# Optimization experiments

Hardware: AMD Instinct MI355X
Metric: run time of the kernel (lower is better)

## Reference

```python
import jax, jax.numpy as jnp
import numpy as np

NUM_HEADS = 16


def setup_inputs() -> dict:
    key = jax.random.key(0)
    ks = jax.random.split(key, 5)
    B, S, E = 4, 2048, 1024
    scale = 1.0 / np.sqrt(E)
    return {
        "x": jax.random.normal(ks[0], (B, S, E), dtype=jnp.float32),
        "w_in": jax.random.normal(ks[1], (E, 3 * E), dtype=jnp.float32) * scale,
        "b_in": jax.random.normal(ks[2], (3 * E,), dtype=jnp.float32) * 0.02,
        "w_out": jax.random.normal(ks[3], (E, E), dtype=jnp.float32) * scale,
        "b_out": jax.random.normal(ks[4], (E,), dtype=jnp.float32) * 0.02,
    }


def reference(x, w_in, b_in, w_out, b_out):
    B, S, E = x.shape
    H = NUM_HEADS
    D = E // H  # head dim
    qkv = x @ w_in + b_in                      # [B,S,3E]
    q, k, v = jnp.split(qkv, 3, axis=-1)       # each [B,S,E]
    q = q.reshape(B, S, H, D)
    k = k.reshape(B, S, H, D)
    v = v.reshape(B, S, H, D)
    # scores scaled by 1/sqrt(D); note: original's causal masked_fill is a
    # no-op (not in-place), so attention is unmasked.
    scores = jnp.einsum("bqhd,bkhd->bhqk", q, k) / jnp.sqrt(jnp.float32(D))
    attn = jax.nn.softmax(scores, axis=-1)      # [B,H,S,S]
    out = jnp.einsum("bhqk,bkhd->bqhd", attn, v).reshape(B, S, E)
    return out @ w_out + b_out
```

## Files before the change

### kernel.cpp

```cpp
#include <hip/hip_runtime.h>
#include <math.h>

#define B_ 4
#define S_ 2048
#define E_ 1024
#define H_ 16
#define D_ 64
#define M_ (B_ * S_)

using f32x4  = __attribute__((ext_vector_type(4))) float;
using short8 = __attribute__((ext_vector_type(8))) short;
using half8  = __attribute__((ext_vector_type(8))) _Float16;
using ushort8_t = __attribute__((ext_vector_type(8))) unsigned short;

__device__ inline unsigned short f2h(float f) {
    _Float16 h = (_Float16)f;
    unsigned short u; __builtin_memcpy(&u, &h, 2); return u;
}
__device__ inline void splith(float f, unsigned short& ho, unsigned short& lo) {
    _Float16 h = (_Float16)f;
    float hf = (float)h;
    _Float16 l = (_Float16)(f - hf);
    __builtin_memcpy(&ho, &h, 2);
    __builtin_memcpy(&lo, &l, 2);
}
__device__ inline unsigned pk2h(float a, float b) {
    auto t = __builtin_amdgcn_cvt_pkrtz(a, b);
    unsigned u; __builtin_memcpy(&u, &t, 4); return u;
}
__device__ inline float ex2(float x) {
#if __has_builtin(__builtin_amdgcn_exp2f)
    return __builtin_amdgcn_exp2f(x);
#else
    return exp2f(x);
#endif
}
__device__ inline f32x4 mfma16(short8 a, short8 b, f32x4 c) {
    half8 ha, hb;
    __builtin_memcpy(&ha, &a, 16);
    __builtin_memcpy(&hb, &b, 16);
    return __builtin_amdgcn_mfma_f32_16x16x32_f16(ha, hb, c, 0, 0, 0);
}
__device__ inline void gload_lds16(const void* g, void* l) {
    __builtin_amdgcn_global_load_lds(
        (const __attribute__((address_space(1))) void*)g,
        (__attribute__((address_space(3))) void*)l, 16, 0, 0);
}

#define QSCALE 0.18033688f

__global__ __launch_bounds__(256)
void split_f16_kernel(const float* __restrict__ X,
                      unsigned short* __restrict__ Xh,
                      unsigned short* __restrict__ Xl)
{
    const size_t i = ((size_t)blockIdx.x * 256 + threadIdx.x) * 4;
    float4 v = *(const float4*)(X + i);
    ushort4 h, l;
    splith(v.x, h.x, l.x);
    splith(v.y, h.y, l.y);
    splith(v.z, h.z, l.z);
    splith(v.w, h.w, l.w);
    *(ushort4*)(Xh + i) = h;
    *(ushort4*)(Xl + i) = l;
}

__global__ __launch_bounds__(256)
void transpose_cvt_kernel(const float* __restrict__ W,
                          unsigned short* __restrict__ Th, int R, int C)
{
    __shared__ float t[32][33];
    const int tx = threadIdx.x & 31, ty = threadIdx.x >> 5;
    const int c0 = blockIdx.x * 32, r0 = blockIdx.y * 32;
    #pragma unroll
    for (int i = 0; i < 4; ++i)
        t[ty + 8 * i][tx] = W[(size_t)(r0 + ty + 8 * i) * C + c0 + tx];
    __syncthreads();
    #pragma unroll
    for (int i = 0; i < 4; ++i) {
        float v = t[tx][ty + 8 * i];
        Th[(size_t)(c0 + ty + 8 * i) * R + r0 + tx] = f2h(v);
    }
}

template<int OUT_MODE>
__global__ __launch_bounds__(256)
void gemm_mfma_kernel(const unsigned short* __restrict__ Ah,
                      const unsigned short* __restrict__ Al,
                      const unsigned short* __restrict__ Bt,
                      const float* __restrict__ bias,
                      float* __restrict__ Cf,
                      unsigned short* __restrict__ Ch,
                      int M, int N, int K)
{
    __shared__ unsigned short AsH[128][64];
    __shared__ unsigned short AsL[128][64];
    __shared__ unsigned short Bs [128][64];

    const int tid  = threadIdx.x;
    const int lane = tid & 63;
    const int wave = tid >> 6;
    const int wm = (wave >> 1) * 64, wn = (wave & 1) * 64;
    const int ln = lane & 15, qd = lane >> 4;
    const int m0 = blockIdx.x * 128, n0 = blockIdx.y * 128;

    f32x4 acc[4][4] = {};

    const int srow_l = lane >> 3;
    const int scol   = ((lane & 7) ^ srow_l) * 8;
    const int swz    = (ln & 7) * 8;

    for (int k0 = 0; k0 < K; k0 += 64) {
        #pragma unroll
        for (int c = 0; c < 4; ++c) {
            const int r = wave * 32 + c * 8;
            const size_t ga = (size_t)(m0 + r + srow_l) * K + k0 + scol;
            const size_t gb = (size_t)(n0 + r + srow_l) * K + k0 + scol;
            gload_lds16(Ah + ga, &AsH[r][0]);
            gload_lds16(Al + ga, &AsL[r][0]);
            gload_lds16(Bt + gb, &Bs [r][0]);
        }
        __syncthreads();

        #pragma unroll
        for (int ks = 0; ks < 2; ++ks) {
            const int co = (ks * 32 + qd * 8) ^ swz;
            short8 ah[4], al[4], bb[4];
            #pragma unroll
            for (int mt = 0; mt < 4; ++mt) {
                ah[mt] = *(const short8*)&AsH[wm + mt * 16 + ln][co];
                al[mt] = *(const short8*)&AsL[wm + mt * 16 + ln][co];
            }
            #pragma unroll
            for (int nt = 0; nt < 4; ++nt)
                bb[nt] = *(const short8*)&Bs[wn + nt * 16 + ln][co];
            __builtin_amdgcn_s_setprio(1);
            #pragma unroll
            for (int mt = 0; mt < 4; ++mt)
                #pragma unroll
                for (int nt = 0; nt < 4; ++nt) {
                    acc[mt][nt] = mfma16(ah[mt], bb[nt], acc[mt][nt]);
                    acc[mt][nt] = mfma16(al[mt], bb[nt], acc[mt][nt]);
                }
            __builtin_amdgcn_s_setprio(0);
        }
        __syncthreads();
    }

    #pragma unroll
    for (int nt = 0; nt < 4; ++nt) {
        const int col = n0 + wn + nt * 16 + ln;
        const float bv = bias[col];
        const float scale = (OUT_MODE == 2 && col < E_) ? QSCALE : 1.0f;
        #pragma unroll
        for (int mt = 0; mt < 4; ++mt) {
            #pragma unroll
            for (int r = 0; r < 4; ++r) {
                const int row = m0 + wm + mt * 16 + qd * 4 + r;
                float f = acc[mt][nt][r] + bv;
                size_t idx = (size_t)row * N + col;
                if (OUT_MODE == 0) Cf[idx] = f;
                else               Ch[idx] = f2h(f * scale);
            }
        }
    }
}

__global__ __launch_bounds__(256)
void attn_mfma_kernel(const unsigned short* __restrict__ qkvh,
                      unsigned short* __restrict__ outh,
                      unsigned short* __restrict__ outl)
{
    constexpr int TQ = 128, TK = 64, LD = 64;
    __shared__ unsigned short Ksh[TK][LD];
    __shared__ unsigned short Vth[D_][LD];
    __shared__ unsigned short Ps[TQ][LD];

    const int tid  = threadIdx.x;
    const int lane = tid & 63;
    const int wave = tid >> 6;
    const int ln = lane & 15, qd = lane >> 4;
    const int id   = blockIdx.x;
    const int g    = id & 63;
    const int qblk = id >> 6;
    const int h    = g & 15;
    const int b    = g >> 4;
    const int wq0 = wave * 32;
    const int swz = (ln & 7) * 8;

    short8 ones8;
    #pragma unroll
    for (int j = 0; j < 8; ++j) ones8[j] = (short)0x3C00;

    short8 qh[2][2];
    #pragma unroll
    for (int qt = 0; qt < 2; ++qt)
        #pragma unroll
        for (int ks = 0; ks < 2; ++ks) {
            size_t base = ((size_t)(b * S_ + qblk * TQ + wq0 + qt * 16 + ln)) * (3 * E_)
                        + h * 64 + ks * 32 + qd * 8;
            qh[qt][ks] = *(const short8*)(qkvh + base);
        }

    f32x4 o[4][2] = {};
    f32x4 ol[2]   = {};

    const int krow = tid >> 2, kcol = (tid & 3) * 16;
    const int kswz = (krow & 7) * 8;
    const int vkey = (tid & 31) * 2, vdc = (tid >> 5) * 8;

    ushort8_t pk0, pk1, pv0, pv1;
    {
        size_t gb = ((size_t)(b * S_ + krow)) * (3 * E_) + E_ + h * 64 + kcol;
        pk0 = *(const ushort8_t*)(qkvh + gb);
        pk1 = *(const ushort8_t*)(qkvh + gb + 8);
        size_t vb0 = ((size_t)(b * S_ + vkey)) * (3 * E_) + 2 * E_ + h * 64 + vdc;
        pv0 = *(const ushort8_t*)(qkvh + vb0);
        pv1 = *(const ushort8_t*)(qkvh + vb0 + 3 * E_);
    }

    for (int kb = 0; kb < S_; kb += TK) {
        *(ushort8_t*)&Ksh[krow][kcol ^ kswz]       = pk0;
        *(ushort8_t*)&Ksh[krow][(kcol + 8) ^ kswz] = pk1;
        #pragma unroll
        for (int j = 0; j < 8; ++j)
            *(unsigned*)&Vth[vdc + j][vkey ^ (j * 8)] =
                (unsigned)pv0[j] | ((unsigned)pv1[j] << 16);
        __syncthreads();

        if (kb + TK < S_) {
            size_t gb = ((size_t)(b * S_ + kb + TK + krow)) * (3 * E_) + E_ + h * 64 + kcol;
            pk0 = *(const ushort8_t*)(qkvh + gb);
            pk1 = *(const ushort8_t*)(qkvh + gb + 8);
            size_t vb0 = ((size_t)(b * S_ + kb + TK + vkey)) * (3 * E_) + 2 * E_ + h * 64 + vdc;
            pv0 = *(const ushort8_t*)(qkvh + vb0);
            pv1 = *(const ushort8_t*)(qkvh + vb0 + 3 * E_);
        }

        f32x4 st[4][2] = {};
        #pragma unroll
        for (int ks = 0; ks < 2; ++ks) {
            const int co = (ks * 32 + qd * 8) ^ swz;
            short8 kh[4];
            #pragma unroll
            for (int kt = 0; kt < 4; ++kt)
                kh[kt] = *(const short8*)&Ksh[kt * 16 + ln][co];
            __builtin_amdgcn_s_setprio(1);
            #pragma unroll
            for (int kt = 0; kt < 4; ++kt)
                #pragma unroll
                for (int qt = 0; qt < 2; ++qt)
                    st[kt][qt] = mfma16(kh[kt], qh[qt][ks], st[kt][qt]);
            __builtin_amdgcn_s_setprio(0);
        }

        const int pswz = (ln & 7) * 8;
        #pragma unroll
        for (int qt = 0; qt < 2; ++qt)
            #pragma unroll
            for (int kt = 0; kt < 4; ++kt) {
                float p0 = ex2(st[kt][qt][0]);
                float p1 = ex2(st[kt][qt][1]);
                float p2 = ex2(st[kt][qt][2]);
                float p3 = ex2(st[kt][qt][3]);
                uint2 w;
                w.x = pk2h(p0, p1);
                w.y = pk2h(p2, p3);
                *(uint2*)&Ps[wq0 + qt * 16 + ln][(kt * 16 + qd * 4) ^ pswz] = w;
            }

        #pragma unroll
        for (int ks = 0; ks < 2; ++ks) {
            const int co = (ks * 32 + qd * 8) ^ swz;
            short8 vA[4], pB[2];
            #pragma unroll
            for (int dt = 0; dt < 4; ++dt)
                vA[dt] = *(const short8*)&Vth[dt * 16 + ln][co];
            #pragma unroll
            for (int qt = 0; qt < 2; ++qt)
                pB[qt] = *(const short8*)&Ps[wq0 + qt * 16 + ln][co];
            __builtin_amdgcn_s_setprio(1);
            #pragma unroll
            for (int dt = 0; dt < 4; ++dt)
                #pragma unroll
                for (int qt = 0; qt < 2; ++qt)
                    o[dt][qt] = mfma16(vA[dt], pB[qt], o[dt][qt]);
            #pragma unroll
            for (int qt = 0; qt < 2; ++qt)
                ol[qt] = mfma16(ones8, pB[qt], ol[qt]);
            __builtin_amdgcn_s_setprio(0);
        }
        __syncthreads();
    }

    float inv[2];
    #pragma unroll
    for (int qt = 0; qt < 2; ++qt)
        inv[qt] = 1.0f / ol[qt][0];
    #pragma unroll
    for (int qt = 0; qt < 2; ++qt) {
        const int q = qblk * TQ + wq0 + qt * 16 + ln;
        #pragma unroll
        for (int dt = 0; dt < 4; ++dt) {
            size_t base = ((size_t)(b * S_ + q)) * E_ + h * 64 + dt * 16 + qd * 4;
            ushort4 hh, ll;
            #pragma unroll
            for (int r = 0; r < 4; ++r) {
                unsigned short h2, l2;
                splith(o[dt][qt][r] * inv[qt], h2, l2);
                ((unsigned short*)&hh)[r] = h2;
                ((unsigned short*)&ll)[r] = l2;
            }
            *(ushort4*)(outh + base) = hh;
            *(ushort4*)(outl + base) = ll;
        }
    }
}

extern "C" void kernel_launch(void* const* d_in, const int* in_sizes, int n_in,
                              void* d_out, int out_size, void* d_ws, size_t ws_size,
                              hipStream_t stream)
{
    const float* x     = (const float*)d_in[0];
    const float* w_in  = (const float*)d_in[1];
    const float* b_in  = (const float*)d_in[2];
    const float* w_out = (const float*)d_in[3];
    const float* b_out = (const float*)d_in[4];
    float* outp = (float*)d_out;

    char* ws = (char*)d_ws;
    unsigned short* qkvh  = (unsigned short*)ws;
    unsigned short* attnh = qkvh  + (size_t)M_ * 3 * E_;
    unsigned short* attnl = attnh + (size_t)M_ * E_;
    unsigned short* xh    = attnl + (size_t)M_ * E_;
    unsigned short* xl    = xh    + (size_t)M_ * E_;
    unsigned short* wInTh  = attnh;
    unsigned short* wOutTh = qkvh;

    split_f16_kernel<<<dim3((M_ * E_) / (4 * 256)), 256, 0, stream>>>(x, xh, xl);

    transpose_cvt_kernel<<<dim3(3 * E_ / 32, E_ / 32), 256, 0, stream>>>(
        w_in, wInTh, E_, 3 * E_);

    gemm_mfma_kernel<2><<<dim3(M_ / 128, (3 * E_) / 128), 256, 0, stream>>>(
        xh, xl, wInTh, b_in, nullptr, qkvh, M_, 3 * E_, E_);

    attn_mfma_kernel<<<dim3((S_ / 128) * H_ * B_), 256, 0, stream>>>(
        qkvh, attnh, attnl);

    transpose_cvt_kernel<<<dim3(E_ / 32, E_ / 32), 256, 0, stream>>>(
        w_out, wOutTh, E_, E_);

    gemm_mfma_kernel<0><<<dim3(M_ / 128, E_ / 128), 256, 0, stream>>>(
        attnh, attnl, wOutTh, b_out, outp, nullptr, M_, E_, E_);
}
```

Baseline: 320.6 us.

## Keep softmax P in registers and double-buffer K/V tiles in attention

Removes the shared-memory staging of the probability tile P by packing the exponentials directly into MFMA B-operand registers, permuting V's key order (vslot) so the register layout matches. K and V are double-buffered in LDS so the next tile is written after compute, dropping one __syncthreads per iteration. This cuts LDS traffic and barrier stalls, at the cost of more LDS for the second K/V buffer and a trickier key permutation that must stay consistent.

Result: slower. 353.9 us (+10.4%).

```diff
diff --git a/kernel.cpp b/kernel.cpp
--- a/kernel.cpp
+++ b/kernel.cpp
@@ -172,9 +172,8 @@
                       unsigned short* __restrict__ outl)
 {
     constexpr int TQ = 128, TK = 64, LD = 64;
-    __shared__ unsigned short Ksh[TK][LD];
-    __shared__ unsigned short Vth[D_][LD];
-    __shared__ unsigned short Ps[TQ][LD];
+    __shared__ unsigned short Ksh[2][TK][LD];
+    __shared__ unsigned short Vth[2][TK][LD];
 
     const int tid  = threadIdx.x;
     const int lane = tid & 63;
@@ -208,6 +207,7 @@
     const int krow = tid >> 2, kcol = (tid & 3) * 16;
     const int kswz = (krow & 7) * 8;
     const int vkey = (tid & 31) * 2, vdc = (tid >> 5) * 8;
+    const int vslot = (vkey & 0x23) | ((vkey & 0x0C) << 1) | ((vkey & 0x10) >> 2);
 
     ushort8_t pk0, pk1, pv0, pv1;
     {
@@ -218,17 +218,19 @@
         pv0 = *(const ushort8_t*)(qkvh + vb0);
         pv1 = *(const ushort8_t*)(qkvh + vb0 + 3 * E_);
     }
-
+    *(ushort8_t*)&Ksh[0][krow][kcol ^ kswz]       = pk0;
+    *(ushort8_t*)&Ksh[0][krow][(kcol + 8) ^ kswz] = pk1;
+    #pragma unroll
+    for (int j = 0; j < 8; ++j)
+        *(unsigned*)&Vth[0][vdc + j][vslot ^ (j * 8)] =
+            (unsigned)pv0[j] | ((unsigned)pv1[j] << 16);
+
+    int cur = 0;
     for (int kb = 0; kb < S_; kb += TK) {
-        *(ushort8_t*)&Ksh[krow][kcol ^ kswz]       = pk0;
-        *(ushort8_t*)&Ksh[krow][(kcol + 8) ^ kswz] = pk1;
-        #pragma unroll
-        for (int j = 0; j < 8; ++j)
-            *(unsigned*)&Vth[vdc + j][vkey ^ (j * 8)] =
-                (unsigned)pv0[j] | ((unsigned)pv1[j] << 16);
         __syncthreads();
 
-        if (kb + TK < S_) {
+        const bool more = (kb + TK < S_);
+        if (more) {
             size_t gb = ((size_t)(b * S_ + kb + TK + krow)) * (3 * E_) + E_ + h * 64 + kcol;
             pk0 = *(const ushort8_t*)(qkvh + gb);
             pk1 = *(const ushort8_t*)(qkvh + gb + 8);
@@ -244,7 +246,7 @@
             short8 kh[4];
             #pragma unroll
             for (int kt = 0; kt < 4; ++kt)
-                kh[kt] = *(const short8*)&Ksh[kt * 16 + ln][co];
+                kh[kt] = *(const short8*)&Ksh[cur][kt * 16 + ln][co];
             __builtin_amdgcn_s_setprio(1);
             #pragma unroll
             for (int kt = 0; kt < 4; ++kt)
@@ -254,43 +256,48 @@
             __builtin_amdgcn_s_setprio(0);
         }
 
-        const int pswz = (ln & 7) * 8;
+        short8 pB[2][2];
         #pragma unroll
         for (int qt = 0; qt < 2; ++qt)
             #pragma unroll
-            for (int kt = 0; kt < 4; ++kt) {
-                float p0 = ex2(st[kt][qt][0]);
-                float p1 = ex2(st[kt][qt][1]);
-                float p2 = ex2(st[kt][qt][2]);
-                float p3 = ex2(st[kt][qt][3]);
-                uint2 w;
-                w.x = pk2h(p0, p1);
-                w.y = pk2h(p2, p3);
-                *(uint2*)&Ps[wq0 + qt * 16 + ln][(kt * 16 + qd * 4) ^ pswz] = w;
+            for (int ks = 0; ks < 2; ++ks) {
+                unsigned w[4];
+                w[0] = pk2h(ex2(st[2 * ks][qt][0]), ex2(st[2 * ks][qt][1]));
+                w[1] = pk2h(ex2(st[2 * ks][qt][2]), ex2(st[2 * ks][qt][3]));
+                w[2] = pk2h(ex2(st[2 * ks + 1][qt][0]), ex2(st[2 * ks + 1][qt][1]));
+                w[3] = pk2h(ex2(st[2 * ks + 1][qt][2]), ex2(st[2 * ks + 1][qt][3]));
+                __builtin_memcpy(&pB[ks][qt], w, 16);
             }
 
         #pragma unroll
         for (int ks = 0; ks < 2; ++ks) {
             const int co = (ks * 32 + qd * 8) ^ swz;
-            short8 vA[4], pB[2];
+            short8 vA[4];
             #pragma unroll
             for (int dt = 0; dt < 4; ++dt)
-                vA[dt] = *(const short8*)&Vth[dt * 16 + ln][co];
-            #pragma unroll
-            for (int qt = 0; qt < 2; ++qt)
-                pB[qt] = *(const short8*)&Ps[wq0 + qt * 16 + ln][co];
+                vA[dt] = *(const short8*)&Vth[cur][dt * 16 + ln][co];
             __builtin_amdgcn_s_setprio(1);
             #pragma unroll
             for (int dt = 0; dt < 4; ++dt)
                 #pragma unroll
                 for (int qt = 0; qt < 2; ++qt)
-                    o[dt][qt] = mfma16(vA[dt], pB[qt], o[dt][qt]);
+                    o[dt][qt] = mfma16(vA[dt], pB[ks][qt], o[dt][qt]);
             #pragma unroll
             for (int qt = 0; qt < 2; ++qt)
-                ol[qt] = mfma16(ones8, pB[qt], ol[qt]);
+                ol[qt] = mfma16(ones8, pB[ks][qt], ol[qt]);
             __builtin_amdgcn_s_setprio(0);
         }
-        __syncthreads();
+
+        if (more) {
+            const int nb = cur ^ 1;
+            *(ushort8_t*)&Ksh[nb][krow][kcol ^ kswz]       = pk0;
+            *(ushort8_t*)&Ksh[nb][krow][(kcol + 8) ^ kswz] = pk1;
+            #pragma unroll
+            for (int j = 0; j < 8; ++j)
+                *(unsigned*)&Vth[nb][vdc + j][vslot ^ (j * 8)] =
+                    (unsigned)pv0[j] | ((unsigned)pv1[j] << 16);
+        }
+        cur ^= 1;
     }
 
     float inv[2];
```
